# Optimization experiments

Measured on AMD Instinct MI355X. Metric: run time of the kernel, lower is better.

## Reference

```python
import jax, jax.numpy as jnp
import numpy as np

H, KV, D, EPS = 32, 8, 128, 1e-6
G = H // KV  # kv groups = 4
ROPE_THETA = 5000000.0


def _rms_norm(x, gamma):
    # x: (..., D)
    return x * jax.lax.rsqrt(jnp.mean(x * x, axis=-1, keepdims=True) + EPS) * gamma


def _rotate_half(x):
    x1, x2 = jnp.split(x, 2, axis=-1)
    return jnp.concatenate([-x2, x1], axis=-1)


def _apply_rope(x, cos, sin):
    # x: (b, h, s, D); cos/sin: (b, s, 1, D) -> (b, 1, s, D)
    cos = jnp.transpose(cos, (0, 2, 1, 3))
    sin = jnp.transpose(sin, (0, 2, 1, 3))
    return x * cos + _rotate_half(x) * sin


def setup_inputs() -> dict:
    key = jax.random.key(0)
    ks = jax.random.split(key, 8)
    b, s, hid = 2, 2048, 2560
    hidden = jax.random.normal(ks[0], (b, s, hid), dtype=jnp.float32)
    # realistic RoPE tables (half-split convention matching _rotate_half)
    inv_freq = 1.0 / (ROPE_THETA ** (np.arange(0, D, 2, dtype=np.float32) / D))  # (D/2,)
    pos = np.arange(s, dtype=np.float32)
    freqs = np.outer(pos, inv_freq)                     # (s, D/2)
    emb = np.concatenate([freqs, freqs], axis=-1)       # (s, D)
    cos = jnp.broadcast_to(jnp.asarray(np.cos(emb))[None, :, None, :], (b, s, 1, D))
    sin = jnp.broadcast_to(jnp.asarray(np.sin(emb))[None, :, None, :], (b, s, 1, D))
    sc = 1.0 / np.sqrt(hid)
    wq = jax.random.normal(ks[1], (H * D, hid), dtype=jnp.float32) * sc
    wk = jax.random.normal(ks[2], (KV * D, hid), dtype=jnp.float32) * sc
    wv = jax.random.normal(ks[3], (KV * D, hid), dtype=jnp.float32) * sc
    wo = jax.random.normal(ks[4], (hid, H * D), dtype=jnp.float32) * (1.0 / np.sqrt(H * D))
    q_gamma = jnp.ones((D,), dtype=jnp.float32)
    k_gamma = jnp.ones((D,), dtype=jnp.float32)
    return {"hidden": hidden, "cos": cos, "sin": sin, "wq": wq, "wk": wk,
            "wv": wv, "wo": wo, "q_gamma": q_gamma, "k_gamma": k_gamma}


def reference(hidden, cos, sin, wq, wk, wv, wo, q_gamma, k_gamma):
    b, s, _ = hidden.shape
    # projections -> (b, heads, s, D)
    q = (hidden @ wq.T).reshape(b, s, H, D).transpose(0, 2, 1, 3)
    k = (hidden @ wk.T).reshape(b, s, KV, D).transpose(0, 2, 1, 3)
    v = (hidden @ wv.T).reshape(b, s, KV, D).transpose(0, 2, 1, 3)
    # QK-RMSNorm over head_dim
    q = _rms_norm(q, q_gamma)
    k = _rms_norm(k, k_gamma)
    # RoPE
    q = _apply_rope(q, cos, sin)
    k = _apply_rope(k, cos, sin)
    new_k, new_v = k, v  # kv cache (no prior cache)
    # GQA attention without materializing expanded K/V
    qg = q.reshape(b, KV, G, s, D)
    scale = 1.0 / np.sqrt(D)
    scores = jnp.einsum('bkgqd,bkld->bkgql', qg, k) * scale  # (b,KV,G,s,s)
    causal = jnp.tril(jnp.ones((s, s), dtype=bool))
    scores = jnp.where(causal, scores, jnp.finfo(scores.dtype).min)
    probs = jax.nn.softmax(scores, axis=-1)
    out = jnp.einsum('bkgql,bkld->bkgqd', probs, v)          # (b,KV,G,s,D)
    out = out.reshape(b, H, s, D).transpose(0, 2, 1, 3).reshape(b, s, H * D)
    return (out @ wo.T, new_k, new_v)
```

## Files before the change

### kernel.cpp

```cpp
#include <hip/hip_runtime.h>
#include <stdint.h>

typedef unsigned short u16;
typedef __attribute__((ext_vector_type(8))) short short8;
typedef __attribute__((ext_vector_type(4))) float f32x4;

#define MFMA_BF16(a,b,c) __builtin_amdgcn_mfma_f32_16x16x32_bf16((a),(b),(c),0,0,0)

#define S_BARRIER()  asm volatile("s_barrier" ::: "memory")
#define WAIT_LGKM0() asm volatile("s_waitcnt lgkmcnt(0)" ::: "memory")
#define WAIT_VM(N)   asm volatile("s_waitcnt vmcnt(" #N ")" ::: "memory")

__device__ __forceinline__ u16 f2bf(float x) {
    uint32_t u = __builtin_bit_cast(uint32_t, x);
    u += 0x7fffu + ((u >> 16) & 1u);
    return (u16)(u >> 16);
}
__device__ __forceinline__ float bf2f(u16 u) {
    return __builtin_bit_cast(float, (uint32_t)u << 16);
}
__device__ __forceinline__ void glds16(const void* g, void* lds) {
    __builtin_amdgcn_global_load_lds((const __attribute__((address_space(1))) void*)g,
                                     (__attribute__((address_space(3))) void*)lds,
                                     16, 0, 0);
}

__device__ __forceinline__ void cvt4(const float* __restrict__ s,
                                     u16* __restrict__ d, int i) {
    float4 v = *(const float4*)(s + i);
    ushort4 o;
    o.x = f2bf(v.x); o.y = f2bf(v.y); o.z = f2bf(v.z); o.w = f2bf(v.w);
    *(ushort4*)(d + i) = o;
}
__global__ __launch_bounds__(256) void cvt_all(
        const float* __restrict__ s0, u16* __restrict__ d0,
        const float* __restrict__ s1, u16* __restrict__ d1,
        const float* __restrict__ s2, u16* __restrict__ d2,
        const float* __restrict__ s3, u16* __restrict__ d3,
        const float* __restrict__ s4, u16* __restrict__ d4)
{
    int i = (blockIdx.x * 256 + threadIdx.x) * 4;
    if      (i < 10485760) cvt4(s0, d0, i);
    else if (i < 20971520) cvt4(s1, d1, i - 10485760);
    else if (i < 23592960) cvt4(s2, d2, i - 20971520);
    else if (i < 26214400) cvt4(s3, d3, i - 23592960);
    else if (i < 36700160) cvt4(s4, d4, i - 26214400);
}

template<int MH, int NH>
__device__ __forceinline__ void mm16(f32x4 (&acc)[8][4],
                                     const short8 (&a)[4][2],
                                     const short8 (&b)[2][2]) {
#pragma unroll
    for (int k2 = 0; k2 < 2; k2++)
#pragma unroll
        for (int mi = 0; mi < 4; mi++)
#pragma unroll
            for (int nj = 0; nj < 2; nj++)
                acc[MH * 4 + mi][NH * 2 + nj] =
                    MFMA_BF16(a[mi][k2], b[nj][k2], acc[MH * 4 + mi][NH * 2 + nj]);
}

template<bool BF16_OUT>
__global__ __launch_bounds__(512, 2) void gemm8(const u16* __restrict__ A,
                                                const u16* __restrict__ B,
                                                void* __restrict__ Cv,
                                                int K, int lda, int ldb, int ldc,
                                                int ntn)
{
    __shared__ __align__(16) u16 Sm[65536];
    const int t = threadIdx.x;
    const int w = t >> 6, l = t & 63;
    const int lrow = l & 15, lk = l >> 4;
    const int wm = w >> 2, wn = w & 3;

    const int nwg = (int)gridDim.x;
    const int cpx = nwg >> 3;
    const int id = (int)blockIdx.x;
    const int sw = (id & 7) * cpx + (id >> 3);
    const int tm = sw / ntn, tn = sw - tm * ntn;
    const int m0 = tm * 256, n0 = tn * 256;

    const int nkt = K >> 6;
    const size_t laneOffA = (size_t)(w * 16 + (l >> 3)) * lda + (((l & 7) ^ (l >> 3)) * 8);
    const size_t laneOffB = (size_t)(w * 16 + (l >> 3)) * ldb + (((l & 7) ^ (l >> 3)) * 8);
    const u16* Ag = A + (size_t)m0 * lda;
    const u16* Bg = B + (size_t)n0 * ldb;

    auto STAGE_A = [&](int kt, int slot, int h) {
#pragma unroll
        for (int j = 0; j < 2; j++)
            glds16(Ag + laneOffA + (size_t)(h * 128 + j * 8) * lda + kt * 64,
                   (char*)Sm + slot * 65536 + h * 16384 + w * 2048 + j * 1024);
    };
    auto STAGE_B = [&](int kt, int slot, int h) {
#pragma unroll
        for (int j = 0; j < 2; j++)
            glds16(Bg + laneOffB + (size_t)(h * 128 + j * 8) * ldb + kt * 64,
                   (char*)Sm + 32768 + slot * 65536 + h * 16384 + w * 2048 + j * 1024);
    };
    auto READ_A = [&](short8 (&a)[4][2], int slot, int rb) {
#pragma unroll
        for (int mi = 0; mi < 4; mi++)
#pragma unroll
            for (int k2 = 0; k2 < 2; k2++) {
                int row = rb + mi * 16 + lrow;
                a[mi][k2] = *(const short8*)&Sm[slot * 32768 + row * 64 +
                                                (((k2 * 4 + lk) ^ (lrow & 7)) * 8)];
            }
    };
    auto READ_B = [&](short8 (&b)[2][2], int slot, int rb) {
#pragma unroll
        for (int nj = 0; nj < 2; nj++)
#pragma unroll
            for (int k2 = 0; k2 < 2; k2++) {
                int row = rb + nj * 16 + lrow;
                b[nj][k2] = *(const short8*)&Sm[slot * 32768 + 16384 + row * 64 +
                                                (((k2 * 4 + lk) ^ (lrow & 7)) * 8)];
            }
    };

    f32x4 acc[8][4];
#pragma unroll
    for (int i = 0; i < 8; i++)
#pragma unroll
        for (int j = 0; j < 4; j++) acc[i][j] = (f32x4){0.f, 0.f, 0.f, 0.f};
    short8 aF0[4][2], aF1[4][2], bF0[2][2], bF1[2][2];

    STAGE_A(0, 0, 0); STAGE_A(0, 0, 1);
    STAGE_B(0, 0, 0); STAGE_B(0, 0, 1);
    const int k1 = (nkt > 1) ? 1 : 0;
    STAGE_A(k1, 1, 0); STAGE_A(k1, 1, 1);
    WAIT_VM(4);
    S_BARRIER();

    for (int kt = 0; kt < nkt; ++kt) {
        const int slot = kt & 1, nslot = slot ^ 1;
        const int ktB = (kt + 1 < nkt) ? kt + 1 : kt;
        const int ktA = (kt + 2 < nkt) ? kt + 2 : kt;
        READ_A(aF0, slot, wm * 128);
        READ_B(bF0, slot, wn * 64);
        STAGE_B(ktB, nslot, 0);
        S_BARRIER();
        WAIT_LGKM0();
        __builtin_amdgcn_sched_barrier(0);
        __builtin_amdgcn_s_setprio(1);
        mm16<0, 0>(acc, aF0, bF0);
        __builtin_amdgcn_s_setprio(0);
        S_BARRIER();
        READ_A(aF1, slot, wm * 128 + 64);
        STAGE_B(ktB, nslot, 1);
        S_BARRIER();
        WAIT_LGKM0();
        __builtin_amdgcn_sched_barrier(0);
        __builtin_amdgcn_s_setprio(1);
        mm16<1, 0>(acc, aF1, bF0);
        __builtin_amdgcn_s_setprio(0);
        S_BARRIER();
        READ_B(bF1, slot, wn * 64 + 32);
        STAGE_A(ktA, slot, 0);
        S_BARRIER();
        WAIT_LGKM0();
        __builtin_amdgcn_sched_barrier(0);
        __builtin_amdgcn_s_setprio(1);
        mm16<1, 1>(acc, aF1, bF1);
        __builtin_amdgcn_s_setprio(0);
        S_BARRIER();
        STAGE_A(ktA, slot, 1);
        S_BARRIER();
        __builtin_amdgcn_s_setprio(1);
        mm16<0, 1>(acc, aF0, bF1);
        __builtin_amdgcn_s_setprio(0);
        WAIT_VM(4);
        S_BARRIER();
    }
    WAIT_VM(0);

#pragma unroll
    for (int mi = 0; mi < 8; mi++) {
#pragma unroll
        for (int r = 0; r < 4; r++) {
            int row = m0 + wm * 128 + mi * 16 + lk * 4 + r;
#pragma unroll
            for (int nj = 0; nj < 4; nj++) {
                int col = n0 + wn * 64 + nj * 16 + lrow;
                float v = acc[mi][nj][r];
                if (BF16_OUT) ((u16*)Cv)[(size_t)row * ldc + col] = f2bf(v);
                else          ((float*)Cv)[(size_t)row * ldc + col] = v;
            }
        }
    }
}

__global__ __launch_bounds__(256) void norm_rope_qk(const u16* __restrict__ qkv,
        const float* __restrict__ cosb, const float* __restrict__ sinb,
        const float* __restrict__ qg, const float* __restrict__ kg,
        u16* __restrict__ qb, u16* __restrict__ kb, float* __restrict__ k_out)
{
    const int idx = blockIdx.x * 4 + (threadIdx.x >> 6);
    const int l = threadIdx.x & 63;
    const int tok = idx / 40, hd = idx - tok * 40;
    const int b = tok >> 11, pos = tok & 2047;
    const u16* row = qkv + (size_t)tok * 6144 + hd * 128;
    float x1 = bf2f(row[l]), x2 = bf2f(row[l + 64]);
    float ss = x1 * x1 + x2 * x2;
#pragma unroll
    for (int m = 1; m < 64; m <<= 1) ss += __shfl_xor(ss, m, 64);
    float rn = rsqrtf(ss * (1.0f / 128.0f) + 1e-6f);

    const float* gm = (hd < 32) ? qg : kg;
    float xn1 = x1 * rn * gm[l];
    float xn2 = x2 * rn * gm[l + 64];
    float c1 = cosb[(size_t)tok * 128 + l],      s1 = sinb[(size_t)tok * 128 + l];
    float c2 = cosb[(size_t)tok * 128 + l + 64], s2 = sinb[(size_t)tok * 128 + l + 64];
    float y1 = xn1 * c1 - xn2 * s1;
    float y2 = xn2 * c2 + xn1 * s2;
    if (hd < 32) {
        const float qs = 0.08838834764831845f;
        size_t base = (((size_t)b * 32 + hd) * 2048 + pos) * 128;
        qb[base + l]      = f2bf(y1 * qs);
        qb[base + l + 64] = f2bf(y2 * qs);
    } else {
        int kv = hd - 32;
        size_t base = (((size_t)b * 8 + kv) * 2048 + pos) * 128;
        k_out[base + l] = y1; k_out[base + l + 64] = y2;
        kb[base + l] = f2bf(y1); kb[base + l + 64] = f2bf(y2);
    }
}

__global__ __launch_bounds__(256) void v_pack(const u16* __restrict__ qkv,
        float* __restrict__ v_out, u16* __restrict__ vtb)
{
    __shared__ __align__(16) u16 T[64 * 128];
    const int pb = blockIdx.x, bkv = blockIdx.y;
    const int b = bkv >> 3, kv = bkv & 7;
    const int p0 = pb * 64;
    const int t = threadIdx.x;
    const int pos = t >> 2, ch4 = t & 3;
    const u16* src = qkv + (size_t)(b * 2048 + p0 + pos) * 6144 + (40 + kv) * 128 + ch4 * 32;
    float* vdst = v_out + ((size_t)bkv * 2048 + p0 + pos) * 128 + ch4 * 32;
#pragma unroll
    for (int j = 0; j < 4; j++) {
        short8 x = *(const short8*)(src + j * 8);
        float4 f0, f1;
        f0.x = bf2f(x[0]); f0.y = bf2f(x[1]); f0.z = bf2f(x[2]); f0.w = bf2f(x[3]);
        f1.x = bf2f(x[4]); f1.y = bf2f(x[5]); f1.z = bf2f(x[6]); f1.w = bf2f(x[7]);
        *(float4*)(vdst + j * 8)     = f0;
        *(float4*)(vdst + j * 8 + 4) = f1;
        int slot = (ch4 * 4 + j) ^ (pos & 7);
        *(short8*)&T[pos * 128 + slot * 8] = x;
    }
    __syncthreads();
    const int d = t & 127, ph = t >> 7;
    u16* obase = vtb + ((size_t)bkv * 128 + d) * 2048 + p0 + ph * 32;
#pragma unroll
    for (int g = 0; g < 4; g++) {
        short8 tv;
#pragma unroll
        for (int jj = 0; jj < 8; jj++) {
            int pp = ph * 32 + g * 8 + jj;
            int slot = (d >> 3) ^ (pp & 7);
            tv[jj] = (short)T[pp * 128 + slot * 8 + (d & 7)];
        }
        *(short8*)(obase + g * 8) = tv;
    }
}

__global__ __launch_bounds__(256, 3) void attn_kernel(const u16* __restrict__ qb,
        const u16* __restrict__ kb, const u16* __restrict__ vtb,
        u16* __restrict__ ao)
{
    __shared__ __align__(16) u16 Ks[64 * 128];
    __shared__ __align__(16) u16 Vs[128 * 64];
    __shared__ __align__(16) u16 Ps[4][32 * 72];

    const int bh = blockIdx.x;
    const int b = bh >> 5, h = bh & 31;
    const int kvh = h >> 2;
    const int qt = (int)gridDim.y - 1 - (int)blockIdx.y;
    const int q0 = qt * 128;
    const int t = threadIdx.x, w = t >> 6, l = t & 63;
    const int lrow = l & 15, lk = l >> 4;

    const u16* qbase  = qb  + ((size_t)b * 32 + h)  * 2048 * 128;
    const u16* kbase  = kb  + ((size_t)b * 8 + kvh) * 2048 * 128;
    const u16* vtbase = vtb + ((size_t)b * 8 + kvh) * 128 * 2048;

    short8 qf[2][4];
#pragma unroll
    for (int m = 0; m < 2; m++) {
        const u16* qrow = qbase + (size_t)(q0 + w * 32 + m * 16 + lrow) * 128 + lk * 8;
#pragma unroll
        for (int ks = 0; ks < 4; ks++) qf[m][ks] = *(const short8*)(qrow + ks * 32);
    }

    f32x4 o[2][8];
#pragma unroll
    for (int m = 0; m < 2; m++)
#pragma unroll
        for (int i = 0; i < 8; i++) o[m][i] = (f32x4){0.f, 0.f, 0.f, 0.f};
    float lsum[2][4] = {{0.f,0.f,0.f,0.f},{0.f,0.f,0.f,0.f}};

    int kR[4], kG[4], vR[4], vG[4];
#pragma unroll
    for (int i = 0; i < 4; i++) {
        int c = i * 256 + t;
        kR[i] = c >> 4; kG[i] = (c & 15) ^ (kR[i] & 7);
        vR[i] = c >> 3; vG[i] = (c & 7)  ^ (vR[i] & 7);
    }
    char* Ksb = (char*)Ks + w * 1024;
    char* Vsb = (char*)Vs + w * 1024;
    u16* pw = &Ps[w][0];
    const int wrow_max = q0 + w * 32 + 31;

    const int nkt = 2 * qt + 2;
    for (int kt = 0; kt < nkt; kt++) {
        const int kv0 = kt * 64;
        __syncthreads();
#pragma unroll
        for (int i = 0; i < 4; i++)
            glds16(kbase + (size_t)(kv0 + kR[i]) * 128 + kG[i] * 8, Ksb + i * 4096);
#pragma unroll
        for (int i = 0; i < 4; i++)
            glds16(vtbase + (size_t)vR[i] * 2048 + kv0 + vG[i] * 8, Vsb + i * 4096);
        __syncthreads();

        if (kv0 > wrow_max) continue;

        f32x4 s[2][4];
#pragma unroll
        for (int m = 0; m < 2; m++)
#pragma unroll
            for (int i = 0; i < 4; i++) s[m][i] = (f32x4){0.f, 0.f, 0.f, 0.f};
#pragma unroll
        for (int ks = 0; ks < 4; ks++) {
#pragma unroll
            for (int nt = 0; nt < 4; nt++) {
                int r = nt * 16 + lrow;
                int sl = (ks * 4 + lk) ^ (r & 7);
                short8 kf = *(const short8*)&Ks[r * 128 + sl * 8];
                s[0][nt] = MFMA_BF16(qf[0][ks], kf, s[0][nt]);
                s[1][nt] = MFMA_BF16(qf[1][ks], kf, s[1][nt]);
            }
        }

#pragma unroll
        for (int m = 0; m < 2; m++) {
            const int rowbase = q0 + w * 32 + m * 16;
            if (kv0 + 63 > rowbase) {
#pragma unroll
                for (int nt = 0; nt < 4; nt++) {
                    int cg = kv0 + nt * 16 + lrow;
#pragma unroll
                    for (int r = 0; r < 4; r++)
                        if (cg > rowbase + lk * 4 + r) s[m][nt][r] = -1e30f;
                }
            }
#pragma unroll
            for (int nt = 0; nt < 4; nt++)
#pragma unroll
                for (int r = 0; r < 4; r++) {
                    float p = __expf(s[m][nt][r]);
                    s[m][nt][r] = p;
                    lsum[m][r] += p;
                    pw[(m * 16 + lk * 4 + r) * 72 + nt * 16 + lrow] = f2bf(p);
                }
        }
        asm volatile("s_waitcnt lgkmcnt(0)" ::: "memory");

#pragma unroll
        for (int k2 = 0; k2 < 2; k2++) {
            short8 pf0 = *(const short8*)&pw[lrow * 72 + k2 * 32 + lk * 8];
            short8 pf1 = *(const short8*)&pw[(16 + lrow) * 72 + k2 * 32 + lk * 8];
#pragma unroll
            for (int nt = 0; nt < 8; nt++) {
                int rr = nt * 16 + lrow;
                int sl = (k2 * 4 + lk) ^ (rr & 7);
                short8 vf = *(const short8*)&Vs[rr * 64 + sl * 8];
                o[0][nt] = MFMA_BF16(pf0, vf, o[0][nt]);
                o[1][nt] = MFMA_BF16(pf1, vf, o[1][nt]);
            }
        }
    }

#pragma unroll
    for (int m = 0; m < 2; m++)
#pragma unroll
        for (int r = 0; r < 4; r++) {
            float v = lsum[m][r];
            v += __shfl_xor(v, 1, 64);
            v += __shfl_xor(v, 2, 64);
            v += __shfl_xor(v, 4, 64);
            v += __shfl_xor(v, 8, 64);
            lsum[m][r] = 1.0f / v;
        }
#pragma unroll
    for (int m = 0; m < 2; m++)
#pragma unroll
        for (int nt = 0; nt < 8; nt++)
#pragma unroll
            for (int r = 0; r < 4; r++) {
                int tok = q0 + w * 32 + m * 16 + lk * 4 + r;
                size_t off = ((size_t)b * 2048 + tok) * 4096 + h * 128 + nt * 16 + lrow;
                ao[off] = f2bf(o[m][nt][r] * lsum[m][r]);
            }
}

extern "C" void kernel_launch(void* const* d_in, const int* in_sizes, int n_in,
                              void* d_out, int out_size, void* d_ws, size_t ws_size,
                              hipStream_t stream)
{
    (void)in_sizes; (void)n_in; (void)out_size; (void)ws_size;
    const float* hidden = (const float*)d_in[0];
    const float* cosb   = (const float*)d_in[1];
    const float* sinb   = (const float*)d_in[2];
    const float* wq     = (const float*)d_in[3];
    const float* wk     = (const float*)d_in[4];
    const float* wv     = (const float*)d_in[5];
    const float* wo     = (const float*)d_in[6];
    const float* qg     = (const float*)d_in[7];
    const float* kg     = (const float*)d_in[8];

    float* out   = (float*)d_out;
    float* k_out = out + (size_t)2 * 2048 * 2560;
    float* v_out = k_out + (size_t)2 * 8 * 2048 * 128;

    u16* hid_b = (u16*)d_ws;
    u16* w_b   = hid_b + 10485760;
    u16* wo_b  = w_b   + 15728640;
    u16* q_b   = wo_b  + 10485760;
    u16* k_b   = q_b   + 16777216;
    u16* vt_b  = k_b   + 4194304;
    u16* qkv_b = vt_b  + 4194304;
    u16* ao_b  = hid_b;

    cvt_all<<<35840, 256, 0, stream>>>(hidden, hid_b, wq, w_b,
                                       wk, w_b + 10485760, wv, w_b + 13107200,
                                       wo, wo_b);

    gemm8<true><<<dim3(384), 512, 0, stream>>>(hid_b, w_b, qkv_b,
                                               2560, 2560, 2560, 6144, 24);
    norm_rope_qk<<<40960, 256, 0, stream>>>(qkv_b, cosb, sinb, qg, kg,
                                            q_b, k_b, k_out);
    v_pack<<<dim3(32, 16), 256, 0, stream>>>(qkv_b, v_out, vt_b);
    attn_kernel<<<dim3(64, 16), 256, 0, stream>>>(q_b, k_b, vt_b, ao_b);
    gemm8<false><<<dim3(160), 512, 0, stream>>>(ao_b, wo_b, out,
                                                4096, 4096, 4096, 2560, 10);
}
```

Baseline: 603.9 us.

## Prefetch next K/V tile during attention compute and fold log2e into Q scale

The attention loop now issues the next tile's K and V global-to-LDS loads while the current tile is being processed. Partial vmcnt waits and split barriers overlap memory traffic with the QK and PV MFMAs, instead of the old load-then-sync-then-compute pattern. The softmax uses exp2f with log2(e) folded into the Q pre-scale. The norm/RoPE kernel switches to paired vector loads and stores, with a lane shuffle supplying the rotate-half partner. The extra barriers and the finer-grained vmcnt bookkeeping add complexity and risk of ordering errors.

```diff
diff --git a/kernel.cpp b/kernel.cpp
--- a/kernel.cpp
+++ b/kernel.cpp
@@ -202,29 +202,34 @@
     const int tok = idx / 40, hd = idx - tok * 40;
     const int b = tok >> 11, pos = tok & 2047;
     const u16* row = qkv + (size_t)tok * 6144 + hd * 128;
-    float x1 = bf2f(row[l]), x2 = bf2f(row[l + 64]);
-    float ss = x1 * x1 + x2 * x2;
+    ushort2 xr = *(const ushort2*)(row + 2 * l);
+    float xa = bf2f(xr.x), xb = bf2f(xr.y);
+    float ss = xa * xa + xb * xb;
 #pragma unroll
     for (int m = 1; m < 64; m <<= 1) ss += __shfl_xor(ss, m, 64);
     float rn = rsqrtf(ss * (1.0f / 128.0f) + 1e-6f);
 
     const float* gm = (hd < 32) ? qg : kg;
-    float xn1 = x1 * rn * gm[l];
-    float xn2 = x2 * rn * gm[l + 64];
-    float c1 = cosb[(size_t)tok * 128 + l],      s1 = sinb[(size_t)tok * 128 + l];
-    float c2 = cosb[(size_t)tok * 128 + l + 64], s2 = sinb[(size_t)tok * 128 + l + 64];
-    float y1 = xn1 * c1 - xn2 * s1;
-    float y2 = xn2 * c2 + xn1 * s2;
+    float2 g = *(const float2*)(gm + 2 * l);
+    float na = xa * rn * g.x, nb = xb * rn * g.y;
+    float pa = __shfl_xor(na, 32, 64);
+    float pb = __shfl_xor(nb, 32, 64);
+    float2 c = *(const float2*)(cosb + (size_t)tok * 128 + 2 * l);
+    float2 s = *(const float2*)(sinb + (size_t)tok * 128 + 2 * l);
+    float sgn = (l < 32) ? -1.0f : 1.0f;
+    float ya = na * c.x + sgn * pa * s.x;
+    float yb = nb * c.y + sgn * pb * s.y;
     if (hd < 32) {
-        const float qs = 0.08838834764831845f;
+        const float qs = 0.12751745f;
         size_t base = (((size_t)b * 32 + hd) * 2048 + pos) * 128;
-        qb[base + l]      = f2bf(y1 * qs);
-        qb[base + l + 64] = f2bf(y2 * qs);
+        ushort2 o; o.x = f2bf(ya * qs); o.y = f2bf(yb * qs);
+        *(ushort2*)(qb + base + 2 * l) = o;
     } else {
         int kv = hd - 32;
         size_t base = (((size_t)b * 8 + kv) * 2048 + pos) * 128;
-        k_out[base + l] = y1; k_out[base + l + 64] = y2;
-        kb[base + l] = f2bf(y1); kb[base + l + 64] = f2bf(y2);
+        *(float2*)(k_out + base + 2 * l) = make_float2(ya, yb);
+        ushort2 o; o.x = f2bf(ya); o.y = f2bf(yb);
+        *(ushort2*)(kb + base + 2 * l) = o;
     }
 }
 
@@ -314,74 +319,97 @@
     const int wrow_max = q0 + w * 32 + 31;
 
     const int nkt = 2 * qt + 2;
+
+#pragma unroll
+    for (int i = 0; i < 4; i++)
+        glds16(kbase + (size_t)kR[i] * 128 + kG[i] * 8, Ksb + i * 4096);
+#pragma unroll
+    for (int i = 0; i < 4; i++)
+        glds16(vtbase + (size_t)vR[i] * 2048 + vG[i] * 8, Vsb + i * 4096);
+
     for (int kt = 0; kt < nkt; kt++) {
         const int kv0 = kt * 64;
-        __syncthreads();
+        const int kvn = ((kt + 1 < nkt) ? kt + 1 : kt) * 64;
+        const bool live = (kv0 <= wrow_max);
+
+        WAIT_VM(4);
+        S_BARRIER();
+
+        f32x4 s[2][4];
+        if (live) {
+#pragma unroll
+            for (int m = 0; m < 2; m++)
+#pragma unroll
+                for (int i = 0; i < 4; i++) s[m][i] = (f32x4){0.f, 0.f, 0.f, 0.f};
+#pragma unroll
+            for (int ks = 0; ks < 4; ks++) {
+#pragma unroll
+                for (int nt = 0; nt < 4; nt++) {
+                    int r = nt * 16 + lrow;
+                    int sl = (ks * 4 + lk) ^ (r & 7);
+                    short8 kf = *(const short8*)&Ks[r * 128 + sl * 8];
+                    s[0][nt] = MFMA_BF16(qf[0][ks], kf, s[0][nt]);
+                    s[1][nt] = MFMA_BF16(qf[1][ks], kf, s[1][nt]);
+                }
+            }
+        }
+        S_BARRIER();
+
 #pragma unroll
         for (int i = 0; i < 4; i++)
-            glds16(kbase + (size_t)(kv0 + kR[i]) * 128 + kG[i] * 8, Ksb + i * 4096);
+            glds16(kbase + (size_t)(kvn + kR[i]) * 128 + kG[i] * 8, Ksb + i * 4096);
+
+        if (live) {
+#pragma unroll
+            for (int m = 0; m < 2; m++) {
+                const int rowbase = q0 + w * 32 + m * 16;
+                if (kv0 + 63 > rowbase) {
+#pragma unroll
+                    for (int nt = 0; nt < 4; nt++) {
+                        int cg = kv0 + nt * 16 + lrow;
+#pragma unroll
+                        for (int r = 0; r < 4; r++)
+                            if (cg > rowbase + lk * 4 + r) s[m][nt][r] = -1e30f;
+                    }
+                }
+#pragma unroll
+                for (int nt = 0; nt < 4; nt++)
+#pragma unroll
+                    for (int r = 0; r < 4; r++) {
+                        float p = exp2f(s[m][nt][r]);
+                        s[m][nt][r] = p;
+                        lsum[m][r] += p;
+                        pw[(m * 16 + lk * 4 + r) * 72 + nt * 16 + lrow] = f2bf(p);
+                    }
+            }
+            WAIT_LGKM0();
+        }
+
+        WAIT_VM(4);
+        S_BARRIER();
+
+        if (live) {
+#pragma unroll
+            for (int k2 = 0; k2 < 2; k2++) {
+                short8 pf0 = *(const short8*)&pw[lrow * 72 + k2 * 32 + lk * 8];
+                short8 pf1 = *(const short8*)&pw[(16 + lrow) * 72 + k2 * 32 + lk * 8];
+#pragma unroll
+                for (int nt = 0; nt < 8; nt++) {
+                    int rr = nt * 16 + lrow;
+                    int sl = (k2 * 4 + lk) ^ (rr & 7);
+                    short8 vf = *(const short8*)&Vs[rr * 64 + sl * 8];
+                    o[0][nt] = MFMA_BF16(pf0, vf, o[0][nt]);
+                    o[1][nt] = MFMA_BF16(pf1, vf, o[1][nt]);
+                }
+            }
+        }
+        S_BARRIER();
+
 #pragma unroll
         for (int i = 0; i < 4; i++)
-            glds16(vtbase + (size_t)vR[i] * 2048 + kv0 + vG[i] * 8, Vsb + i * 4096);
-        __syncthreads();
-
-        if (kv0 > wrow_max) continue;
-
-        f32x4 s[2][4];
-#pragma unroll
-        for (int m = 0; m < 2; m++)
-#pragma unroll
-            for (int i = 0; i < 4; i++) s[m][i] = (f32x4){0.f, 0.f, 0.f, 0.f};
-#pragma unroll
-        for (int ks = 0; ks < 4; ks++) {
-#pragma unroll
-            for (int nt = 0; nt < 4; nt++) {
-                int r = nt * 16 + lrow;
-                int sl = (ks * 4 + lk) ^ (r & 7);
-                short8 kf = *(const short8*)&Ks[r * 128 + sl * 8];
-                s[0][nt] = MFMA_BF16(qf[0][ks], kf, s[0][nt]);
-                s[1][nt] = MFMA_BF16(qf[1][ks], kf, s[1][nt]);
-            }
-        }
-
-#pragma unroll
-        for (int m = 0; m < 2; m++) {
-            const int rowbase = q0 + w * 32 + m * 16;
-            if (kv0 + 63 > rowbase) {
-#pragma unroll
-                for (int nt = 0; nt < 4; nt++) {
-                    int cg = kv0 + nt * 16 + lrow;
-#pragma unroll
-                    for (int r = 0; r < 4; r++)
-                        if (cg > rowbase + lk * 4 + r) s[m][nt][r] = -1e30f;
-                }
-            }
-#pragma unroll
-            for (int nt = 0; nt < 4; nt++)
-#pragma unroll
-                for (int r = 0; r < 4; r++) {
-                    float p = __expf(s[m][nt][r]);
-                    s[m][nt][r] = p;
-                    lsum[m][r] += p;
-                    pw[(m * 16 + lk * 4 + r) * 72 + nt * 16 + lrow] = f2bf(p);
-                }
-        }
-        asm volatile("s_waitcnt lgkmcnt(0)" ::: "memory");
-
-#pragma unroll
-        for (int k2 = 0; k2 < 2; k2++) {
-            short8 pf0 = *(const short8*)&pw[lrow * 72 + k2 * 32 + lk * 8];
-            short8 pf1 = *(const short8*)&pw[(16 + lrow) * 72 + k2 * 32 + lk * 8];
-#pragma unroll
-            for (int nt = 0; nt < 8; nt++) {
-                int rr = nt * 16 + lrow;
-                int sl = (k2 * 4 + lk) ^ (rr & 7);
-                short8 vf = *(const short8*)&Vs[rr * 64 + sl * 8];
-                o[0][nt] = MFMA_BF16(pf0, vf, o[0][nt]);
-                o[1][nt] = MFMA_BF16(pf1, vf, o[1][nt]);
-            }
-        }
-    }
+            glds16(vtbase + (size_t)vR[i] * 2048 + kvn + vG[i] * 8, Vsb + i * 4096);
+    }
+    WAIT_VM(0);
 
 #pragma unroll
     for (int m = 0; m < 2; m++)
```

New measurement: 660.2 us. 9.3% more time.
